# Optimization experiments

Hardware: AMD Instinct MI355X
Metric: run time of the kernel (lower is better)

## Reference

```python
import jax, jax.numpy as jnp
import numpy as np

DIM = 1024
NUM_HEADS = 16
HEAD_DIM = DIM // NUM_HEADS
EPS_NORM = 1e-12  # F.normalize eps
EPS_LN = 1e-5     # nn.LayerNorm eps


def setup_inputs() -> dict:
    key = jax.random.key(0)
    ks = jax.random.split(key, 6)
    x = jax.random.normal(ks[0], (4, 2048, DIM), dtype=jnp.float32)
    # LayerNorm params
    ln_w = jnp.ones((DIM,), jnp.float32)
    ln_b = jnp.zeros((DIM,), jnp.float32)
    # qkv: xavier_uniform on weight [3D, D], zero bias
    limit = float(np.sqrt(6.0 / (DIM + 3 * DIM)))
    qkv_w = jax.random.uniform(ks[1], (3 * DIM, DIM), jnp.float32, -limit, limit)
    qkv_b = jnp.zeros((3 * DIM,), jnp.float32)
    # out_proj: normal std=0.02, zero bias
    out_w = 0.02 * jax.random.normal(ks[2], (DIM, DIM), dtype=jnp.float32)
    out_b = jnp.zeros((DIM,), jnp.float32)
    return {"x": x, "ln_w": ln_w, "ln_b": ln_b, "qkv_w": qkv_w,
            "qkv_b": qkv_b, "out_w": out_w, "out_b": out_b}


def reference(x, ln_w, ln_b, qkv_w, qkv_b, out_w, out_b):
    B, N, D = x.shape
    # pre-LayerNorm
    mu = jnp.mean(x, axis=-1, keepdims=True)
    var = jnp.mean(jnp.square(x - mu), axis=-1, keepdims=True)
    h = (x - mu) / jnp.sqrt(var + EPS_LN) * ln_w + ln_b
    # QKV projection (torch Linear: y = h @ W^T + b)
    qkv = h @ qkv_w.T + qkv_b                     # [B, N, 3D]
    qkv = qkv.reshape(B, N, 3, NUM_HEADS, HEAD_DIM)
    q, k, v = (jnp.transpose(qkv[:, :, i], (0, 2, 1, 3)) for i in range(3))  # [B,H,N,hd]
    # per-head L2 normalize (F.normalize semantics: x / max(||x||, eps))
    q = q / jnp.maximum(jnp.linalg.norm(q, axis=-1, keepdims=True), EPS_NORM)
    k = k / jnp.maximum(jnp.linalg.norm(k, axis=-1, keepdims=True), EPS_NORM)
    scale = HEAD_DIM ** 0.5
    attn = jnp.einsum('bhqd,bhkd->bhqk', q, k) * scale
    attn = jax.nn.softmax(attn, axis=-1)
    out = jnp.einsum('bhqk,bhkd->bhqd', attn, v)  # [B,H,N,hd]
    out = jnp.transpose(out, (0, 2, 1, 3)).reshape(B, N, D)
    return x + out @ out_w.T + out_b
```

## Files before the change

### kernel.cpp

```cpp
#include <hip/hip_runtime.h>
#include <math.h>

constexpr int D     = 1024;
constexpr int NH    = 16;
constexpr int HD    = 64;
constexpr int SEQ   = 2048;
constexpr int BATCH = 4;
constexpr int NTOK  = BATCH * SEQ;

typedef short s16x8 __attribute__((ext_vector_type(8)));
typedef short s16x4 __attribute__((ext_vector_type(4)));
typedef float f32x4 __attribute__((ext_vector_type(4)));
typedef unsigned short u16;
typedef unsigned int   u32;

#if __has_builtin(__builtin_amdgcn_exp2f)
#define EXP2(x) __builtin_amdgcn_exp2f(x)
#else
#define EXP2(x) exp2f(x)
#endif

__device__ __forceinline__ short f2bf(float f) {
    unsigned u = __float_as_uint(f);
    unsigned r = (u + 0x7FFFu + ((u >> 16) & 1u)) >> 16;
    return (short)r;
}
__device__ __forceinline__ float bf2f(u16 s) {
    return __uint_as_float(((unsigned)s) << 16);
}

__device__ __forceinline__ u32 pack_bf16_pair(float f0, float f1) {
    u32 a = __float_as_uint(f1) + 0x8000u;
    u32 b = __float_as_uint(f0) + 0x8000u;
    return __builtin_amdgcn_perm(a, b, 0x07060302u);
}

__device__ __forceinline__ void async_lds16(const void* g, void* l) {
    __builtin_amdgcn_global_load_lds(
        (const __attribute__((address_space(1))) unsigned int*)g,
        (__attribute__((address_space(3))) unsigned int*)l, 16, 0, 0);
}

__device__ __forceinline__ float block_reduce_sum(float v, float* red) {
    int lane = threadIdx.x & 63, wid = threadIdx.x >> 6;
    #pragma unroll
    for (int off = 32; off > 0; off >>= 1) v += __shfl_down(v, off, 64);
    if (lane == 0) red[wid] = v;
    __syncthreads();
    float r = red[0] + red[1] + red[2] + red[3];
    __syncthreads();
    return r;
}

__global__ __launch_bounds__(256) void ln_kernel(const float* __restrict__ x,
                                                 const float* __restrict__ w,
                                                 const float* __restrict__ b,
                                                 u16* __restrict__ h) {
    __shared__ float red[4];
    int row = blockIdx.x;
    const float* xr = x + (size_t)row * D;
    int t = threadIdx.x;
    float v[4];
    float s = 0.f;
    #pragma unroll
    for (int i = 0; i < 4; i++) { v[i] = xr[t + 256 * i]; s += v[i]; }
    float mean = block_reduce_sum(s, red) * (1.0f / 1024.0f);
    float ss = 0.f;
    #pragma unroll
    for (int i = 0; i < 4; i++) { float d = v[i] - mean; ss += d * d; }
    float var = block_reduce_sum(ss, red) * (1.0f / 1024.0f);
    float rstd = rsqrtf(var + 1e-5f);
    u16* hr = h + (size_t)row * D;
    #pragma unroll
    for (int i = 0; i < 4; i++) {
        int c = t + 256 * i;
        hr[c] = (u16)f2bf((v[i] - mean) * rstd * w[c] + b[c]);
    }
}

__global__ __launch_bounds__(256) void cast_kernel(const float* __restrict__ in,
                                                   u16* __restrict__ out, int n) {
    int i = (blockIdx.x * 256 + threadIdx.x) * 4;
    if (i >= n) return;
    float4 f = *(const float4*)(in + i);
    s16x4 o4;
    o4[0] = f2bf(f.x); o4[1] = f2bf(f.y); o4[2] = f2bf(f.z); o4[3] = f2bf(f.w);
    *(s16x4*)(out + i) = o4;
}

__device__ __forceinline__ s16x8 rdfrag(const u16* lds, int row, int kk, int quad) {
    int byte = row * 128 + ((kk * 64 + quad * 16) ^ ((row & 7) << 4));
    return *(const s16x8*)((const char*)lds + byte);
}

__device__ __forceinline__ void stage_half_A(const u16* __restrict__ A, u16* ldsA,
                                             int rowBase, int K, int kt, int hs,
                                             int wave, int lane) {
    #pragma unroll
    for (int i = 0; i < 2; i++) {
        int c = wave * 2 + i;
        int baserow = ((c & 7) * 8) + ((c >> 3) << 7) + (hs << 6);
        int row = baserow + (lane >> 3);
        int colb = ((lane & 7) * 16) ^ ((row & 7) << 4);
        const u16* src = A + (size_t)(rowBase + row) * K + kt * 64 + (colb >> 1);
        async_lds16(src, ldsA + baserow * 64);
    }
}
__device__ __forceinline__ void stage_half_B(const u16* __restrict__ B, u16* ldsB,
                                             int colBase, int K, int kt, int hs,
                                             int wave, int lane) {
    #pragma unroll
    for (int i = 0; i < 2; i++) {
        int c = wave * 2 + i;
        int baserow = ((c & 3) * 8) + ((c >> 2) << 6) + (hs << 5);
        int row = baserow + (lane >> 3);
        int colb = ((lane & 7) * 16) ^ ((row & 7) << 4);
        const u16* src = B + (size_t)(colBase + row) * K + kt * 64 + (colb >> 1);
        async_lds16(src, ldsB + baserow * 64);
    }
}

template <typename OutT, bool RES, bool NORMK>
__global__ __launch_bounds__(512, 2) void gemm256(const u16* __restrict__ A,
                                                  const u16* __restrict__ B,
                                                  const float* __restrict__ bias,
                                                  const float* __restrict__ R,
                                                  OutT* __restrict__ C,
                                                  int M, int N, int K) {
    __shared__ u16 lds[2][2][256 * 64];

    int nby = M >> 8;
    int cpx = gridDim.x >> 3;
    int bid = blockIdx.x;
    int swz = (bid & 7) * cpx + (bid >> 3);
    int bx = swz / nby, by = swz % nby;
    int rowBase = by << 8, colBase = bx << 8;

    int tid = threadIdx.x, wave = tid >> 6, lane = tid & 63;
    int quad = lane >> 4, l16 = lane & 15;
    int wr = wave >> 2, wc = wave & 3;
    int KT = K >> 6;

    f32x4 acc[8][4];
    #pragma unroll
    for (int m = 0; m < 8; m++)
        #pragma unroll
        for (int n = 0; n < 4; n++)
            acc[m][n] = (f32x4){0.f, 0.f, 0.f, 0.f};

    stage_half_A(A, &lds[0][0][0], rowBase, K, 0, 0, wave, lane);
    stage_half_B(B, &lds[0][1][0], colBase, K, 0, 0, wave, lane);
    stage_half_A(A, &lds[0][0][0], rowBase, K, 0, 1, wave, lane);
    stage_half_B(B, &lds[0][1][0], colBase, K, 0, 1, wave, lane);
    stage_half_A(A, &lds[1][0][0], rowBase, K, 1, 0, wave, lane);
    stage_half_B(B, &lds[1][1][0], colBase, K, 1, 0, wave, lane);
    stage_half_A(A, &lds[1][0][0], rowBase, K, 1, 1, wave, lane);
    asm volatile("s_waitcnt vmcnt(6)" ::: "memory");
    __builtin_amdgcn_s_barrier();

    for (int t = 0; t < KT; ++t) {
        int bsel = t & 1;
        u16* cA = &lds[bsel][0][0];
        u16* cB = &lds[bsel][1][0];
        u16* oB = &lds[bsel ^ 1][1][0];
        int t1 = t + 1; if (t1 >= KT) t1 -= KT;
        int t2 = t + 2; if (t2 >= KT) t2 -= KT;

        s16x8 af[4][2], bf0[2][2], bf1[2][2];

        #pragma unroll
        for (int m = 0; m < 4; m++)
            #pragma unroll
            for (int kk = 0; kk < 2; kk++)
                af[m][kk] = rdfrag(cA, wr * 128 + m * 16 + l16, kk, quad);
        #pragma unroll
        for (int n = 0; n < 2; n++)
            #pragma unroll
            for (int kk = 0; kk < 2; kk++)
                bf0[n][kk] = rdfrag(cB, wc * 64 + n * 16 + l16, kk, quad);
        stage_half_B(B, oB, colBase, K, t1, 1, wave, lane);
        __builtin_amdgcn_s_barrier();
        __builtin_amdgcn_s_setprio(1);
        #pragma unroll
        for (int kk = 0; kk < 2; kk++)
            #pragma unroll
            for (int m = 0; m < 4; m++)
                #pragma unroll
                for (int n = 0; n < 2; n++)
                    acc[m][n] = __builtin_amdgcn_mfma_f32_16x16x32_bf16(
                        af[m][kk], bf0[n][kk], acc[m][n], 0, 0, 0);
        __builtin_amdgcn_s_setprio(0);
        __builtin_amdgcn_s_barrier();

        #pragma unroll
        for (int n = 0; n < 2; n++)
            #pragma unroll
            for (int kk = 0; kk < 2; kk++)
                bf1[n][kk] = rdfrag(cB, wc * 64 + (n + 2) * 16 + l16, kk, quad);
        stage_half_A(A, cA, rowBase, K, t2, 0, wave, lane);
        __builtin_amdgcn_s_barrier();
        __builtin_amdgcn_s_setprio(1);
        #pragma unroll
        for (int kk = 0; kk < 2; kk++)
            #pragma unroll
            for (int m = 0; m < 4; m++)
                #pragma unroll
                for (int n = 0; n < 2; n++)
                    acc[m][n + 2] = __builtin_amdgcn_mfma_f32_16x16x32_bf16(
                        af[m][kk], bf1[n][kk], acc[m][n + 2], 0, 0, 0);
        __builtin_amdgcn_s_setprio(0);
        __builtin_amdgcn_s_barrier();

        #pragma unroll
        for (int m = 0; m < 4; m++)
            #pragma unroll
            for (int kk = 0; kk < 2; kk++)
                af[m][kk] = rdfrag(cA, wr * 128 + (m + 4) * 16 + l16, kk, quad);
        stage_half_B(B, cB, colBase, K, t2, 0, wave, lane);
        __builtin_amdgcn_s_barrier();
        __builtin_amdgcn_s_setprio(1);
        #pragma unroll
        for (int kk = 0; kk < 2; kk++)
            #pragma unroll
            for (int m = 0; m < 4; m++)
                #pragma unroll
                for (int n = 0; n < 2; n++)
                    acc[m + 4][n] = __builtin_amdgcn_mfma_f32_16x16x32_bf16(
                        af[m][kk], bf0[n][kk], acc[m + 4][n], 0, 0, 0);
        __builtin_amdgcn_s_setprio(0);
        __builtin_amdgcn_s_barrier();

        stage_half_A(A, cA, rowBase, K, t2, 1, wave, lane);
        __builtin_amdgcn_s_barrier();
        __builtin_amdgcn_s_setprio(1);
        #pragma unroll
        for (int kk = 0; kk < 2; kk++)
            #pragma unroll
            for (int m = 0; m < 4; m++)
                #pragma unroll
                for (int n = 0; n < 2; n++)
                    acc[m + 4][n + 2] = __builtin_amdgcn_mfma_f32_16x16x32_bf16(
                        af[m][kk], bf1[n][kk], acc[m + 4][n + 2], 0, 0, 0);
        __builtin_amdgcn_s_setprio(0);
        asm volatile("s_waitcnt vmcnt(6)" ::: "memory");
        __builtin_amdgcn_s_barrier();
    }
    asm volatile("s_waitcnt vmcnt(0)" ::: "memory");

    bool normk = NORMK && (colBase + wc * 64) >= 1024 && (colBase + wc * 64) < 2048;

    #pragma unroll
    for (int m = 0; m < 8; m++) {
        float vals[4][4];
        #pragma unroll
        for (int n = 0; n < 4; n++) {
            int gn = colBase + wc * 64 + n * 16 + l16;
            float bv = bias[gn];
            #pragma unroll
            for (int r = 0; r < 4; r++) {
                float val = acc[m][n][r] + bv;
                if (RES) {
                    int gm = rowBase + wr * 128 + m * 16 + quad * 4 + r;
                    val += R[(size_t)gm * N + gn];
                }
                vals[n][r] = val;
            }
        }
        if (normk) {
            #pragma unroll
            for (int r = 0; r < 4; r++) {
                float ssq = 0.f;
                #pragma unroll
                for (int n = 0; n < 4; n++) ssq = fmaf(vals[n][r], vals[n][r], ssq);
                ssq += __shfl_xor(ssq, 1, 64);
                ssq += __shfl_xor(ssq, 2, 64);
                ssq += __shfl_xor(ssq, 4, 64);
                ssq += __shfl_xor(ssq, 8, 64);
                float inv = 1.0f / fmaxf(sqrtf(ssq), 1e-12f);
                #pragma unroll
                for (int n = 0; n < 4; n++) vals[n][r] *= inv;
            }
        }
        #pragma unroll
        for (int n = 0; n < 4; n++) {
            int gn = colBase + wc * 64 + n * 16 + l16;
            int gm0 = rowBase + wr * 128 + m * 16 + quad * 4;
            #pragma unroll
            for (int r = 0; r < 4; r++) {
                if constexpr (sizeof(OutT) == 2)
                    C[(size_t)(gm0 + r) * N + gn] = (OutT)f2bf(vals[n][r]);
                else
                    C[(size_t)(gm0 + r) * N + gn] = vals[n][r];
            }
        }
    }
}

__global__ __launch_bounds__(256, 2) void mha_kernel(const u16* __restrict__ qkv,
                                                     u16* __restrict__ out) {
    __shared__ u16 Ks[64 * 64];
    constexpr int VS = 68;
    __shared__ u16 Vt[64 * VS];

    int bh = blockIdx.x & 63;
    int qt = blockIdx.x >> 6;
    int b  = bh >> 4, h = bh & 15;
    int tid = threadIdx.x;
    int wave = tid >> 6, lane = tid & 63;
    int quad = lane >> 4, l16 = lane & 15;

    const size_t rs = 3072;
    constexpr float SCL = 11.5415605f;

    s16x8 aq[4][2];
    #pragma unroll
    for (int rt = 0; rt < 4; rt++) {
        const u16* qb = qkv + ((size_t)(b * SEQ) + qt * 256 + wave * 64 + rt * 16 + l16) * rs + h * 64;
        s16x8 r0 = *(const s16x8*)(qb + quad * 8);
        s16x8 r1 = *(const s16x8*)(qb + 32 + quad * 8);
        float f0[8], f1[8], ss = 0.f;
        #pragma unroll
        for (int i = 0; i < 8; i++) { f0[i] = bf2f((u16)r0[i]); ss = fmaf(f0[i], f0[i], ss); }
        #pragma unroll
        for (int i = 0; i < 8; i++) { f1[i] = bf2f((u16)r1[i]); ss = fmaf(f1[i], f1[i], ss); }
        ss += __shfl_xor(ss, 16, 64);
        ss += __shfl_xor(ss, 32, 64);
        float inv = SCL / fmaxf(sqrtf(ss), 1e-12f);
        #pragma unroll
        for (int i = 0; i < 8; i++) {
            aq[rt][0][i] = f2bf(f0[i] * inv);
            aq[rt][1][i] = f2bf(f1[i] * inv);
        }
    }

    const f32x4 cinit = {-SCL, -SCL, -SCL, -SCL};
    f32x4 o2[4][4];
    f32x4 osum[4];
    #pragma unroll
    for (int rt = 0; rt < 4; rt++) {
        #pragma unroll
        for (int ht = 0; ht < 4; ht++) o2[rt][ht] = (f32x4){0.f, 0.f, 0.f, 0.f};
        osum[rt] = (f32x4){0.f, 0.f, 0.f, 0.f};
    }
    s16x8 ones;
    #pragma unroll
    for (int i = 0; i < 8; i++) ones[i] = (short)0x3F80;

    int skey = tid >> 2, c4 = tid & 3;
    int ksw  = skey & 7;
    int vp2 = tid >> 3, dc = (tid & 7) * 8;
    const u16* kglob  = qkv + ((size_t)(b * SEQ) + skey) * rs + 1024 + h * 64 + c4 * 16;
    const u16* vglob0 = qkv + ((size_t)(b * SEQ) + 2 * vp2) * rs + 2048 + h * 64 + dc;
    u16* kdst0 = &Ks[skey * 64 + ((2 * c4)     ^ ksw) * 8];
    u16* kdst1 = &Ks[skey * 64 + ((2 * c4 + 1) ^ ksw) * 8];
    u32* vt32 = (u32*)&Vt[0];

    s16x8 kr0 = ((const s16x8*)kglob)[0];
    s16x8 kr1 = ((const s16x8*)kglob)[1];
    s16x8 vr0 = *(const s16x8*)(vglob0);
    s16x8 vr1 = *(const s16x8*)(vglob0 + rs);

    int swz = l16 & 7;

    for (int kb = 0; kb < SEQ / 64; kb++) {
        __syncthreads();
        *(s16x8*)kdst0 = kr0;
        *(s16x8*)kdst1 = kr1;
        #pragma unroll
        for (int i = 0; i < 8; i++) {
            u32 pk = (u32)(u16)vr0[i] | ((u32)(u16)vr1[i] << 16);
            vt32[(dc + i) * (VS / 2) + vp2] = pk;
        }
        __syncthreads();

        if (kb < SEQ / 64 - 1) {
            const u16* kp = kglob + (size_t)(kb + 1) * 64 * rs;
            const u16* vp = vglob0 + (size_t)(kb + 1) * 64 * rs;
            kr0 = ((const s16x8*)kp)[0];
            kr1 = ((const s16x8*)kp)[1];
            vr0 = *(const s16x8*)(vp);
            vr1 = *(const s16x8*)(vp + rs);
        }

        s16x4 pfr[4][4];
        #pragma unroll
        for (int t = 0; t < 4; t++) {
            const u16* krow = &Ks[(t * 16 + l16) * 64];
            s16x8 bk0 = *(const s16x8*)(krow + ((0 + quad) ^ swz) * 8);
            s16x8 bk1 = *(const s16x8*)(krow + ((4 + quad) ^ swz) * 8);
            #pragma unroll
            for (int rt = 0; rt < 4; rt++) {
                f32x4 s = cinit;
                s = __builtin_amdgcn_mfma_f32_16x16x32_bf16(bk0, aq[rt][0], s, 0, 0, 0);
                s = __builtin_amdgcn_mfma_f32_16x16x32_bf16(bk1, aq[rt][1], s, 0, 0, 0);
                uint2 pk2;
                pk2.x = pack_bf16_pair(EXP2(s[0]), EXP2(s[1]));
                pk2.y = pack_bf16_pair(EXP2(s[2]), EXP2(s[3]));
                pfr[rt][t] = __builtin_bit_cast(s16x4, pk2);
            }
        }

        #pragma unroll
        for (int pr = 0; pr < 2; pr++) {
            int tA = pr * 2, tB = pr * 2 + 1;
            s16x8 bp[4];
            #pragma unroll
            for (int rt = 0; rt < 4; rt++)
                bp[rt] = __builtin_shufflevector(pfr[rt][tA], pfr[rt][tB],
                                                 0, 1, 2, 3, 4, 5, 6, 7);
            #pragma unroll
            for (int ht = 0; ht < 4; ht++) {
                const u16* vrow = &Vt[(ht * 16 + l16) * VS];
                s16x4 va = *(const s16x4*)(vrow + tA * 16 + quad * 4);
                s16x4 vb = *(const s16x4*)(vrow + tB * 16 + quad * 4);
                s16x8 vfr = __builtin_shufflevector(va, vb, 0, 1, 2, 3, 4, 5, 6, 7);
                #pragma unroll
                for (int rt = 0; rt < 4; rt++)
                    o2[rt][ht] = __builtin_amdgcn_mfma_f32_16x16x32_bf16(
                        vfr, bp[rt], o2[rt][ht], 0, 0, 0);
            }
            #pragma unroll
            for (int rt = 0; rt < 4; rt++)
                osum[rt] = __builtin_amdgcn_mfma_f32_16x16x32_bf16(
                    ones, bp[rt], osum[rt], 0, 0, 0);
        }
    }

    #pragma unroll
    for (int rt = 0; rt < 4; rt++) {
        float inv = 1.0f / osum[rt][0];
        int orow = b * SEQ + qt * 256 + wave * 64 + rt * 16 + l16;
        u16* op = out + (size_t)orow * D + h * 64 + quad * 4;
        #pragma unroll
        for (int ht = 0; ht < 4; ht++) {
            f32x4 v = o2[rt][ht];
            u32 lo = pack_bf16_pair(v[0] * inv, v[1] * inv);
            u32 hi = pack_bf16_pair(v[2] * inv, v[3] * inv);
            uint2 pk = {lo, hi};
            *(uint2*)(op + ht * 16) = pk;
        }
    }
}

extern "C" void kernel_launch(void* const* d_in, const int* in_sizes, int n_in,
                              void* d_out, int out_size, void* d_ws, size_t ws_size,
                              hipStream_t stream) {
    const float* x     = (const float*)d_in[0];
    const float* ln_w  = (const float*)d_in[1];
    const float* ln_b  = (const float*)d_in[2];
    const float* qkv_w = (const float*)d_in[3];
    const float* qkv_b = (const float*)d_in[4];
    const float* out_w = (const float*)d_in[5];
    const float* out_b = (const float*)d_in[6];
    float* y = (float*)d_out;

    char* ws = (char*)d_ws;
    u16* qkv = (u16*)ws;
    u16* h   = (u16*)(ws + (size_t)48 * 1024 * 1024);
    u16* wq  = (u16*)(ws + (size_t)64 * 1024 * 1024);
    u16* wo  = (u16*)(ws + (size_t)70 * 1024 * 1024);
    u16* attn_out = h;

    ln_kernel<<<NTOK, 256, 0, stream>>>(x, ln_w, ln_b, h);
    cast_kernel<<<(3 * D * D) / 1024, 256, 0, stream>>>(qkv_w, wq, 3 * D * D);
    cast_kernel<<<(D * D) / 1024, 256, 0, stream>>>(out_w, wo, D * D);

    gemm256<u16, false, true><<<(3 * D / 256) * (NTOK / 256), 512, 0, stream>>>(
        h, wq, qkv_b, nullptr, qkv, NTOK, 3 * D, D);

    mha_kernel<<<BATCH * NH * (SEQ / 256), 256, 0, stream>>>(qkv, attn_out);

    gemm256<float, true, false><<<(D / 256) * (NTOK / 256), 512, 0, stream>>>(
        attn_out, wo, out_b, x, y, NTOK, D, D);
}
```

Baseline: 290.1 us.

## Double-buffer K/V tiles in attention and swap QKV GEMM for 128x128 kernel

```diff
diff --git a/kernel.cpp b/kernel.cpp
--- a/kernel.cpp
+++ b/kernel.cpp
@@ -88,6 +88,105 @@
     *(s16x4*)(out + i) = o4;
 }
 
+template <typename OutT, bool RES, bool NORMK>
+__global__ __launch_bounds__(256) void gemm_bf16(const u16* __restrict__ A,
+                                                 const u16* __restrict__ B,
+                                                 const float* __restrict__ bias,
+                                                 const float* __restrict__ R,
+                                                 OutT* __restrict__ C,
+                                                 int M, int N, int K) {
+    __shared__ u16 As[128 * 32];
+    __shared__ u16 Bs[128 * 32];
+    int tid = threadIdx.x, wave = tid >> 6, lane = tid & 63;
+    int quad = lane >> 4, l16 = lane & 15;
+    int wm = (wave & 1) * 64, wn = (wave >> 1) * 64;
+    int rowBase = blockIdx.y * 128, colBase = blockIdx.x * 128;
+
+    int srow = lane >> 2;
+    int sk8  = (lane & 3) * 8;
+
+    f32x4 acc[4][4];
+    #pragma unroll
+    for (int i = 0; i < 4; i++)
+        #pragma unroll
+        for (int j = 0; j < 4; j++)
+            acc[i][j] = (f32x4){0.f, 0.f, 0.f, 0.f};
+
+    for (int k0 = 0; k0 < K; k0 += 32) {
+        __syncthreads();
+        #pragma unroll
+        for (int i = 0; i < 2; i++) {
+            int r = wave * 32 + i * 16;
+            const u16* ga = A + (size_t)(rowBase + r + srow) * K + k0 + sk8;
+            async_lds16(ga, &As[r * 32]);
+            const u16* gb = B + (size_t)(colBase + r + srow) * K + k0 + sk8;
+            async_lds16(gb, &Bs[r * 32]);
+        }
+        __syncthreads();
+
+        s16x8 af[4], bfr[4];
+        #pragma unroll
+        for (int t = 0; t < 4; t++) {
+            af[t]  = *(const s16x8*)&As[(wm + t * 16 + l16) * 32 + quad * 8];
+            bfr[t] = *(const s16x8*)&Bs[(wn + t * 16 + l16) * 32 + quad * 8];
+        }
+        #pragma unroll
+        for (int mt = 0; mt < 4; mt++)
+            #pragma unroll
+            for (int nt = 0; nt < 4; nt++)
+                acc[mt][nt] = __builtin_amdgcn_mfma_f32_16x16x32_bf16(
+                    af[mt], bfr[nt], acc[mt][nt], 0, 0, 0);
+    }
+
+    bool normk = NORMK && (colBase + wn) >= 1024 && (colBase + wn) < 2048;
+
+    #pragma unroll
+    for (int mt = 0; mt < 4; mt++) {
+        float vals[4][4];
+        #pragma unroll
+        for (int nt = 0; nt < 4; nt++) {
+            int gn = colBase + wn + nt * 16 + l16;
+            float bv = bias[gn];
+            #pragma unroll
+            for (int r = 0; r < 4; r++) {
+                float val = acc[mt][nt][r] + bv;
+                if (RES) {
+                    int gm = rowBase + wm + mt * 16 + quad * 4 + r;
+                    val += R[(size_t)gm * N + gn];
+                }
+                vals[nt][r] = val;
+            }
+        }
+        if (normk) {
+            #pragma unroll
+            for (int r = 0; r < 4; r++) {
+                float ssq = 0.f;
+                #pragma unroll
+                for (int nt = 0; nt < 4; nt++) ssq = fmaf(vals[nt][r], vals[nt][r], ssq);
+                ssq += __shfl_xor(ssq, 1, 64);
+                ssq += __shfl_xor(ssq, 2, 64);
+                ssq += __shfl_xor(ssq, 4, 64);
+                ssq += __shfl_xor(ssq, 8, 64);
+                float inv = 1.0f / fmaxf(sqrtf(ssq), 1e-12f);
+                #pragma unroll
+                for (int nt = 0; nt < 4; nt++) vals[nt][r] *= inv;
+            }
+        }
+        #pragma unroll
+        for (int nt = 0; nt < 4; nt++) {
+            int gn = colBase + wn + nt * 16 + l16;
+            int gm0 = rowBase + wm + mt * 16 + quad * 4;
+            #pragma unroll
+            for (int r = 0; r < 4; r++) {
+                if constexpr (sizeof(OutT) == 2)
+                    C[(size_t)(gm0 + r) * N + gn] = (OutT)f2bf(vals[nt][r]);
+                else
+                    C[(size_t)(gm0 + r) * N + gn] = vals[nt][r];
+            }
+        }
+    }
+}
+
 __device__ __forceinline__ s16x8 rdfrag(const u16* lds, int row, int kk, int quad) {
     int byte = row * 128 + ((kk * 64 + quad * 16) ^ ((row & 7) << 4));
     return *(const s16x8*)((const char*)lds + byte);
@@ -298,9 +397,9 @@
 
 __global__ __launch_bounds__(256, 2) void mha_kernel(const u16* __restrict__ qkv,
                                                      u16* __restrict__ out) {
-    __shared__ u16 Ks[64 * 64];
+    __shared__ u16 Ks[2][64 * 64];
     constexpr int VS = 68;
-    __shared__ u16 Vt[64 * VS];
+    __shared__ u16 Vt[2][64 * VS];
 
     int bh = blockIdx.x & 63;
     int qt = blockIdx.x >> 6;
@@ -351,9 +450,8 @@
     int vp2 = tid >> 3, dc = (tid & 7) * 8;
     const u16* kglob  = qkv + ((size_t)(b * SEQ) + skey) * rs + 1024 + h * 64 + c4 * 16;
     const u16* vglob0 = qkv + ((size_t)(b * SEQ) + 2 * vp2) * rs + 2048 + h * 64 + dc;
-    u16* kdst0 = &Ks[skey * 64 + ((2 * c4)     ^ ksw) * 8];
-    u16* kdst1 = &Ks[skey * 64 + ((2 * c4 + 1) ^ ksw) * 8];
-    u32* vt32 = (u32*)&Vt[0];
+    int koff0 = skey * 64 + ((2 * c4)     ^ ksw) * 8;
+    int koff1 = skey * 64 + ((2 * c4 + 1) ^ ksw) * 8;
 
     s16x8 kr0 = ((const s16x8*)kglob)[0];
     s16x8 kr1 = ((const s16x8*)kglob)[1];
@@ -363,9 +461,13 @@
     int swz = l16 & 7;
 
     for (int kb = 0; kb < SEQ / 64; kb++) {
-        __syncthreads();
-        *(s16x8*)kdst0 = kr0;
-        *(s16x8*)kdst1 = kr1;
+        int bsel = kb & 1;
+        u16* ksb = &Ks[bsel][0];
+        u16* vtb = &Vt[bsel][0];
+
+        *(s16x8*)(ksb + koff0) = kr0;
+        *(s16x8*)(ksb + koff1) = kr1;
+        u32* vt32 = (u32*)vtb;
         #pragma unroll
         for (int i = 0; i < 8; i++) {
             u32 pk = (u32)(u16)vr0[i] | ((u32)(u16)vr1[i] << 16);
@@ -385,7 +487,7 @@
         s16x4 pfr[4][4];
         #pragma unroll
         for (int t = 0; t < 4; t++) {
-            const u16* krow = &Ks[(t * 16 + l16) * 64];
+            const u16* krow = ksb + (t * 16 + l16) * 64;
             s16x8 bk0 = *(const s16x8*)(krow + ((0 + quad) ^ swz) * 8);
             s16x8 bk1 = *(const s16x8*)(krow + ((4 + quad) ^ swz) * 8);
             #pragma unroll
@@ -410,7 +512,7 @@
                                                  0, 1, 2, 3, 4, 5, 6, 7);
             #pragma unroll
             for (int ht = 0; ht < 4; ht++) {
-                const u16* vrow = &Vt[(ht * 16 + l16) * VS];
+                const u16* vrow = vtb + (ht * 16 + l16) * VS;
                 s16x4 va = *(const s16x4*)(vrow + tA * 16 + quad * 4);
                 s16x4 vb = *(const s16x4*)(vrow + tB * 16 + quad * 4);
                 s16x8 vfr = __builtin_shufflevector(va, vb, 0, 1, 2, 3, 4, 5, 6, 7);
@@ -465,8 +567,11 @@
     cast_kernel<<<(3 * D * D) / 1024, 256, 0, stream>>>(qkv_w, wq, 3 * D * D);
     cast_kernel<<<(D * D) / 1024, 256, 0, stream>>>(out_w, wo, D * D);
 
-    gemm256<u16, false, true><<<(3 * D / 256) * (NTOK / 256), 512, 0, stream>>>(
-        h, wq, qkv_b, nullptr, qkv, NTOK, 3 * D, D);
+    {
+        dim3 grid(3 * D / 128, NTOK / 128);
+        gemm_bf16<u16, false, true><<<grid, 256, 0, stream>>>(h, wq, qkv_b, nullptr,
+                                                              qkv, NTOK, 3 * D, D);
+    }
 
     mha_kernel<<<BATCH * NH * (SEQ / 256), 256, 0, stream>>>(qkv, attn_out);
 
```

After: 298.8 us. +3.0%, slower.
